# Optimization experiments

Measured on AMD Instinct MI355X. Metric: run time of the kernel, lower is better.

Reference implementation:

```python
import jax, jax.numpy as jnp
import numpy as np

BINS = 256          # bins_per_sample (== embedding_dim, required by the module's math)
NUM_EMB = 256       # num_embeddings
EMB_DIM = 256       # embedding_dim
# dropout_prob = 0.1 -> identity in eval mode (reference runs deterministic/eval)


def setup_inputs() -> dict:
    key = jax.random.key(0)
    k1, k2 = jax.random.split(key)
    sequence_embeddings = jax.random.normal(k1, (2, 4, BINS, EMB_DIM), dtype=jnp.float32)
    emb_table = jax.random.normal(k2, (NUM_EMB, EMB_DIM), dtype=jnp.float32)
    return {"sequence_embeddings": sequence_embeddings, "emb_table": emb_table}


def reference(sequence_embeddings, emb_table):
    # relative-distance index: |i - j| clamped to [0, NUM_EMB-1]  -> [bins, bins]
    idx = jnp.arange(BINS)
    dist_idx = jnp.clip(jnp.abs(idx[:, None] - idx[None, :]), 0, NUM_EMB - 1)
    dist_embed = emb_table[dist_idx]                      # [bins, bins, d]

    # x1[..., i, j, d] = x[..., j, d];  x2[..., i, j, d] = x[..., i, d]
    x1 = sequence_embeddings[..., None, :, :]             # [..., 1,    bins, d]
    x2 = sequence_embeddings[..., :, None, :]             # [..., bins, 1,    d]

    # (x1 + x2)/2 + x1*x2 + distance embedding (dropout = identity in eval)
    return (x1 + x2) * 0.5 + x1 * x2 + dist_embed
```

## Files before the change

kernel.cpp:

```cpp
#include <hip/hip_runtime.h>

#define BINS 256
#define EMB  256
#define BH   8

__global__ __launch_bounds__(256) void outputhead_kernel(
        const float* __restrict__ seq,
        const float* __restrict__ tab,
        float* __restrict__ out)
{
    const int blk = blockIdx.x;
    const int bh  = blk >> 8;
    const int i   = blk & 255;
    const int t   = threadIdx.x;
    const int d4  = t & 63;
    const int tj  = t >> 6;

    const float4* __restrict__ seq4 = reinterpret_cast<const float4*>(seq);
    const float4* __restrict__ tab4 = reinterpret_cast<const float4*>(tab);
    float4* __restrict__ out4       = reinterpret_cast<float4*>(out);

    const float4 si = seq4[(bh * BINS + i) * (EMB / 4) + d4];

    const size_t seq_bh_base  = (size_t)bh * BINS * (EMB / 4);
    const size_t out_row_base = ((size_t)(bh * BINS + i)) * BINS * (EMB / 4);

    #pragma unroll 4
    for (int jb = 0; jb < BINS; jb += 4) {
        const int j    = jb + tj;
        const int dist = (i > j) ? (i - j) : (j - i);

        const float4 sj = seq4[seq_bh_base + (size_t)j * (EMB / 4) + d4];
        const float4 tv = tab4[(size_t)dist * (EMB / 4) + d4];

        float4 o;
        o.x = (si.x + sj.x) * 0.5f + si.x * sj.x + tv.x;
        o.y = (si.y + sj.y) * 0.5f + si.y * sj.y + tv.y;
        o.z = (si.z + sj.z) * 0.5f + si.z * sj.z + tv.z;
        o.w = (si.w + sj.w) * 0.5f + si.w * sj.w + tv.w;

        out4[out_row_base + (size_t)j * (EMB / 4) + d4] = o;
    }
}

extern "C" void kernel_launch(void* const* d_in, const int* in_sizes, int n_in,
                              void* d_out, int out_size, void* d_ws, size_t ws_size,
                              hipStream_t stream) {
    const float* seq = (const float*)d_in[0];
    const float* tab = (const float*)d_in[1];
    float* out = (float*)d_out;

    dim3 grid(BH * BINS);
    dim3 block(256);
    outputhead_kernel<<<grid, block, 0, stream>>>(seq, tab, out);
}
```

Baseline: 110.1 us.

## Exploit output symmetry in i,j and pair rows for balanced blocks

```diff
diff --git a/kernel.cpp b/kernel.cpp
--- a/kernel.cpp
+++ b/kernel.cpp
@@ -1,56 +1,58 @@
 #include <hip/hip_runtime.h>
 
 #define BINS 256
-#define EMB  256
+#define EMBV 64
 #define BH   8
 
-__global__ __launch_bounds__(256) void outputhead_kernel(
-        const float* __restrict__ seq,
-        const float* __restrict__ tab,
-        float* __restrict__ out)
+typedef float f32x4 __attribute__((ext_vector_type(4)));
+
+__global__ __launch_bounds__(512) void outputhead_sym(
+        const f32x4* __restrict__ seq4,
+        const f32x4* __restrict__ tab4,
+        f32x4* __restrict__ out4)
 {
     const int blk = blockIdx.x;
-    const int bh  = blk >> 8;
-    const int i   = blk & 255;
+    const int bh  = blk >> 7;
+    const int b   = blk & 127;
     const int t   = threadIdx.x;
     const int d4  = t & 63;
     const int tj  = t >> 6;
 
-    const float4* __restrict__ seq4 = reinterpret_cast<const float4*>(seq);
-    const float4* __restrict__ tab4 = reinterpret_cast<const float4*>(tab);
-    float4* __restrict__ out4       = reinterpret_cast<float4*>(out);
+    const size_t seq_base = (size_t)bh * BINS * EMBV;
+    const size_t out_bh   = (size_t)bh * BINS * BINS * EMBV;
 
-    const float4 si = seq4[(bh * BINS + i) * (EMB / 4) + d4];
+    #pragma unroll
+    for (int r = 0; r < 2; ++r) {
+        const int i = (r == 0) ? b : (BINS - 1 - b);
+        const f32x4 si = seq4[seq_base + (size_t)i * EMBV + d4];
+        const size_t out_row_i = out_bh + (size_t)i * BINS * EMBV;
 
-    const size_t seq_bh_base  = (size_t)bh * BINS * (EMB / 4);
-    const size_t out_row_base = ((size_t)(bh * BINS + i)) * BINS * (EMB / 4);
+        for (int jb = 0; jb <= i; jb += 8) {
+            const int j = jb + tj;
+            if (j > i) break;
 
-    #pragma unroll 4
-    for (int jb = 0; jb < BINS; jb += 4) {
-        const int j    = jb + tj;
-        const int dist = (i > j) ? (i - j) : (j - i);
+            const f32x4 sj = seq4[seq_base + (size_t)j * EMBV + d4];
+            const f32x4 tv = tab4[(size_t)(i - j) * EMBV + d4];
 
-        const float4 sj = seq4[seq_bh_base + (size_t)j * (EMB / 4) + d4];
-        const float4 tv = tab4[(size_t)dist * (EMB / 4) + d4];
+            const f32x4 o = (si + sj) * 0.5f + si * sj + tv;
 
-        float4 o;
-        o.x = (si.x + sj.x) * 0.5f + si.x * sj.x + tv.x;
-        o.y = (si.y + sj.y) * 0.5f + si.y * sj.y + tv.y;
-        o.z = (si.z + sj.z) * 0.5f + si.z * sj.z + tv.z;
-        o.w = (si.w + sj.w) * 0.5f + si.w * sj.w + tv.w;
-
-        out4[out_row_base + (size_t)j * (EMB / 4) + d4] = o;
+            __builtin_nontemporal_store(o, &out4[out_row_i + (size_t)j * EMBV + d4]);
+            if (j != i) {
+                __builtin_nontemporal_store(
+                    o, &out4[out_bh + (size_t)j * BINS * EMBV + (size_t)i * EMBV + d4]);
+            }
+        }
     }
 }
 
 extern "C" void kernel_launch(void* const* d_in, const int* in_sizes, int n_in,
                               void* d_out, int out_size, void* d_ws, size_t ws_size,
                               hipStream_t stream) {
-    const float* seq = (const float*)d_in[0];
-    const float* tab = (const float*)d_in[1];
-    float* out = (float*)d_out;
+    const f32x4* seq4 = (const f32x4*)d_in[0];
+    const f32x4* tab4 = (const f32x4*)d_in[1];
+    f32x4* out4 = (f32x4*)d_out;
 
-    dim3 grid(BH * BINS);
-    dim3 block(256);
-    outputhead_kernel<<<grid, block, 0, stream>>>(seq, tab, out);
+    dim3 grid(BH * 128);
+    dim3 block(512);
+    outputhead_sym<<<grid, block, 0, stream>>>(seq4, tab4, out4);
 }
```

Result: slower. 114.6 us (+4.1%).
